# Optimization experiments

Measured on AMD Instinct MI355X. Metric: run time of the kernel, lower is better.

## Reference

```python
import jax, jax.numpy as jnp
import numpy as np

CONF = 0.25      # confidence threshold (module default)
IOU = 0.45       # NMS IoU threshold (class attribute)
TOPK = 1000      # fixed candidate budget (jit-friendly stand-in for boolean filtering)
MAX_WH = 4096.0  # class offset so NMS is per-class (YOLOv5 trick)


def xywh2xyxy(b):
    xy, wh = b[..., :2], b[..., 2:4]
    return jnp.concatenate([xy - wh * 0.5, xy + wh * 0.5], axis=-1)


def box_iou(a, b):
    # a: [K,4] xyxy, b: [K,4] xyxy -> [K,K]
    lt = jnp.maximum(a[:, None, :2], b[None, :, :2])
    rb = jnp.minimum(a[:, None, 2:], b[None, :, 2:])
    wh = jnp.clip(rb - lt, 0.0)
    inter = wh[..., 0] * wh[..., 1]
    area_a = (a[:, 2] - a[:, 0]) * (a[:, 3] - a[:, 1])
    area_b = (b[:, 2] - b[:, 0]) * (b[:, 3] - b[:, 1])
    return inter / (area_a[:, None] + area_b[None, :] - inter + 1e-9)


def nms_single(pred):
    # pred: [N, 5+C] = (xywh, obj, cls scores)
    boxes = xywh2xyxy(pred[:, :4])
    obj = pred[:, 4]
    cls = pred[:, 5:]
    cls_conf = jnp.max(cls, axis=-1)
    cls_id = jnp.argmax(cls, axis=-1)
    score = obj * cls_conf                       # conf = obj_conf * cls_conf
    masked = jnp.where(score > CONF, score, -1.0)
    top_scores, idx = jax.lax.top_k(masked, TOPK)  # sorted descending
    boxes_k = boxes[idx]                          # [K,4]
    cls_k = cls_id[idx].astype(boxes.dtype)       # [K]
    valid_k = top_scores > CONF                   # candidates passing threshold
    # per-class NMS via coordinate offset
    off = boxes_k + cls_k[:, None] * MAX_WH
    iou = box_iou(off, off)
    iou = iou * (1.0 - jnp.eye(TOPK, dtype=iou.dtype))  # ignore self-IoU
    # greedy suppression in descending score order
    def step(suppressed, i):
        keep_i = jnp.logical_and(jnp.logical_not(suppressed[i]), valid_k[i])
        suppressed = jnp.logical_or(suppressed, jnp.logical_and(keep_i, iou[i] > IOU))
        return suppressed, keep_i
    _, keep = jax.lax.scan(step, jnp.zeros(TOPK, dtype=bool), jnp.arange(TOPK))
    det = jnp.concatenate([boxes_k, top_scores[:, None], cls_k[:, None]], axis=-1)  # [K,6]
    return jnp.where(keep[:, None], det, 0.0)


def setup_inputs() -> dict:
    key = jax.random.key(0)
    x = jax.random.uniform(key, (8, 25200, 85), dtype=jnp.float32)
    return {"x": x}


def reference(x):
    # [B, K, 6] detections (xyxy, conf, cls); suppressed/invalid rows zeroed.
    return jax.vmap(nms_single)(x)
```

## Files before the change

kernel.cpp:

```cpp
#include <hip/hip_runtime.h>
#include <stdint.h>

#define NB 8
#define NPRED 25200
#define NTOP 1000
#define NCLS 80
#define CONF_T 0.25f
#define IOU_THR 0.45f
#define MAXWH 4096.0f
#define CAP 2048
#define NBINS2 8192
#define SBLK 128
#define SBPB 197

typedef unsigned long long u64;

__device__ __forceinline__ u64 shfl_xor_u64(u64 v, int m) {
    int lo = __shfl_xor((int)(unsigned)v, m);
    int hi = __shfl_xor((int)(unsigned)(v >> 32), m);
    return ((u64)(unsigned)hi << 32) | (unsigned)lo;
}
__device__ __forceinline__ u64 shfl_u64(u64 v, int src) {
    int lo = __shfl((int)(unsigned)v, src);
    int hi = __shfl((int)(unsigned)(v >> 32), src);
    return ((u64)(unsigned)hi << 32) | (unsigned)lo;
}

__global__ __launch_bounds__(256) void k_score(const float* __restrict__ x,
                                               float* __restrict__ msc,
                                               int* __restrict__ cls) {
#pragma clang fp contract(off)
    __shared__ __align__(16) float sm[SBLK * 85];
    const int b = blockIdx.x / SBPB;
    const int blk = blockIdx.x % SBPB;
    const int t = threadIdx.x;
    const int wave = t >> 6, lane = t & 63;
    const long long TOT4 = (long long)NB * NPRED * 85 / 4;
    const long long base4 = ((long long)b * NPRED + (long long)blk * SBLK) * 85 / 4;
    const float4* x4 = (const float4*)x;
    const int tile4 = SBLK * 85 / 4;

    for (int k = 0; k < 11; ++k) {
        int ib = k * 256 + wave * 64;
        int fi = ib + lane;
        if (fi < tile4) {
            long long gi = base4 + fi;
            if (gi >= TOT4) gi = TOT4 - 1;
            __builtin_amdgcn_global_load_lds(
                (const __attribute__((address_space(1))) void*)(x4 + gi),
                (__attribute__((address_space(3))) void*)(sm + (size_t)ib * 4),
                16, 0, 0);
        }
    }
    __syncthreads();

    const int p = t >> 1;
    const int h = t & 1;
    const int pred = blk * SBLK + p;
    const float* rowp = &sm[p * 85];
    float obj = rowp[4];
    const int cb = 5 + h * 40;
    float best = rowp[cb];
    int bid = h * 40;
    for (int c = 1; c < 40; ++c) {
        float v = rowp[cb + c];
        if (v > best) { best = v; bid = h * 40 + c; }
    }
    float obest = __shfl_xor(best, 1);
    int obid = __shfl_xor(bid, 1);
    if (h == 0 && pred < NPRED) {
        float fb = best; int fc = bid;
        if (obest > fb) { fb = obest; fc = obid; }
        float score = obj * fb;
        int q = b * NPRED + pred;
        msc[q] = (score > CONF_T) ? score : -1.0f;
        cls[q] = fc;
    }
}

__global__ __launch_bounds__(1024) void k_fused(const float* __restrict__ x,
                                                const float* __restrict__ msc,
                                                const int* __restrict__ cls,
                                                float* __restrict__ out) {
#pragma clang fp contract(off)
    __shared__ __align__(16) unsigned char uni[CAP * 8];
    __shared__ __align__(16) unsigned hh[NBINS2];
    __shared__ __align__(16) float4 obx[NTOP];
    __shared__ float oco[NTOP];
    __shared__ float osc[NTOP];
    __shared__ int   ocl[NTOP];
    __shared__ int sB;
    __shared__ unsigned lcnt;
    __shared__ int ovf;
    u64* keys = (u64*)uni;
    const int b = blockIdx.x, t = threadIdx.x;
    const float* ms = msc + (size_t)b * NPRED;

    float sv[25];
#pragma unroll
    for (int k = 0; k < 25; ++k) {
        int p = t + k * 1024;
        sv[k] = (p < NPRED) ? ms[p] : -1.0f;
    }

    for (int i = t; i < NBINS2; i += 1024) hh[i] = 0;
    if (t == 0) { lcnt = 0; ovf = 0; sB = 0; }
    __syncthreads();

#pragma unroll
    for (int k = 0; k < 25; ++k) {
        float s = sv[k];
        if (s > CONF_T) {
            unsigned bits = __float_as_uint(s);
            int bin = (int)(bits >> 11) - 0x7D000;
            bin = bin < 0 ? 0 : (bin > 8191 ? 8191 : bin);
            atomicAdd(&hh[bin], 1u);
        }
    }
    __syncthreads();

    unsigned* ctmp = (unsigned*)uni;
    {
        const uint4* h4 = (const uint4*)hh;
        uint4 a = h4[t * 2], d = h4[t * 2 + 1];
        ctmp[t] = a.x + a.y + a.z + a.w + d.x + d.y + d.z + d.w;
    }
    __syncthreads();

    if (t < 64) {
        const int lane = t;
        const int hi = 1023 - 16 * lane;
        unsigned lc[16];
        unsigned sum = 0;
#pragma unroll
        for (int k = 0; k < 16; ++k) { lc[k] = ctmp[hi - k]; sum += lc[k]; }
        unsigned v = sum;
        for (int d = 1; d < 64; d <<= 1) {
            unsigned o = __shfl_up(v, d);
            if (lane >= d) v += o;
        }
        unsigned excl = v - sum;
        u64 ball = __ballot(v >= NTOP);
        if (ball != 0) {
            int sel = __builtin_ctzll(ball);
            if (lane == sel) {
                unsigned run = excl, runBefore = 0;
                int C = 0;
                for (int k = 0; k < 16; ++k) {
                    runBefore = run;
                    run += lc[k];
                    if (run >= NTOP) { C = hi - k; break; }
                }
                const uint4* f4 = (const uint4*)&hh[C * 8];
                uint4 fa = f4[0], fb = f4[1];
                unsigned fbin[8] = {fa.x, fa.y, fa.z, fa.w, fb.x, fb.y, fb.z, fb.w};
                unsigned run2 = runBefore;
                int Bf = C * 8;
                for (int ff = 7; ff >= 0; --ff) {
                    run2 += fbin[ff];
                    if (run2 >= NTOP) { Bf = C * 8 + ff; break; }
                }
                sB = Bf;
            }
        }
    }
    __syncthreads();
    const int B = sB;

#pragma unroll
    for (int k = 0; k < 25; ++k) {
        float s = sv[k];
        if (s > CONF_T) {
            unsigned bits = __float_as_uint(s);
            int bin = (int)(bits >> 11) - 0x7D000;
            bin = bin < 0 ? 0 : (bin > 8191 ? 8191 : bin);
            if (bin >= B) {
                unsigned slot = atomicAdd(&lcnt, 1u);
                if (slot < CAP)
                    keys[slot] = ((u64)(~bits) << 32) | (unsigned)(t + k * 1024);
            }
        }
    }
    __syncthreads();
    unsigned c = lcnt; if (c > CAP) c = CAP;
    const bool fastSort = (c <= 1024u);
    const unsigned PAD = fastSort ? 1024u : (unsigned)CAP;
    for (unsigned i = c + t; i < PAD; i += 1024) keys[i] = ~0ULL;
    __syncthreads();

    if (fastSort) {
        u64 v = keys[t];
        for (unsigned k = 2; k <= 64; k <<= 1)
            for (unsigned j = k >> 1; j >= 1; j >>= 1) {
                u64 pv = shfl_xor_u64(v, (int)j);
                bool asc = (((unsigned)t & k) == 0u);
                bool lower = (((unsigned)t & j) == 0u);
                bool tm = (asc == lower);
                v = ((v < pv) == tm) ? v : pv;
            }
        for (unsigned k = 128; k <= 1024; k <<= 1) {
            for (unsigned j = k >> 1; j >= 64; j >>= 1) {
                keys[t] = v;
                __syncthreads();
                u64 pv = keys[(unsigned)t ^ j];
                bool asc = (((unsigned)t & k) == 0u);
                bool lower = (((unsigned)t & j) == 0u);
                bool tm = (asc == lower);
                v = ((v < pv) == tm) ? v : pv;
                __syncthreads();
            }
            for (unsigned j = 32; j >= 1; j >>= 1) {
                u64 pv = shfl_xor_u64(v, (int)j);
                bool asc = (((unsigned)t & k) == 0u);
                bool lower = (((unsigned)t & j) == 0u);
                bool tm = (asc == lower);
                v = ((v < pv) == tm) ? v : pv;
            }
        }
        keys[t] = v;
        __syncthreads();
    } else {
        const unsigned ia = (((unsigned)t & ~63u) << 1) | ((unsigned)t & 63u);
        const unsigned ib = ia + 64u;
        auto ce = [&](u64& v, unsigned i, unsigned j, unsigned k) {
            u64 pv = shfl_xor_u64(v, (int)j);
            bool asc = ((i & k) == 0u);
            bool lower = ((i & j) == 0u);
            bool takeMin = (asc == lower);
            bool less = (v < pv);
            v = (takeMin == less) ? v : pv;
        };
        {
            u64 a = keys[ia], d = keys[ib];
            for (unsigned k = 2; k <= 64; k <<= 1)
                for (unsigned j = k >> 1; j >= 1; j >>= 1) {
                    ce(a, ia, j, k);
                    ce(d, ib, j, k);
                }
            keys[ia] = a; keys[ib] = d;
        }
        __syncthreads();
        for (unsigned k = 128; k <= CAP; k <<= 1) {
            for (unsigned j = k >> 1; j >= 64; j >>= 1) {
                unsigned i = (((unsigned)t & ~(j - 1)) << 1) | ((unsigned)t & (j - 1));
                unsigned pi = i | j;
                bool up = ((i & k) == 0);
                u64 a = keys[i], d = keys[pi];
                bool sw = up ? (a > d) : (a < d);
                if (sw) { keys[i] = d; keys[pi] = a; }
                __syncthreads();
            }
            u64 a = keys[ia], d = keys[ib];
            for (unsigned j = 32; j >= 1; j >>= 1) {
                ce(a, ia, j, k);
                ce(d, ib, j, k);
            }
            keys[ia] = a; keys[ib] = d;
            __syncthreads();
        }
    }

    if (t < NTOP) {
        u64 key = keys[t];
        unsigned p = (unsigned)key;
        float score = __uint_as_float(~(unsigned)(key >> 32));
        bool v = score > CONF_T;
        float4 o = make_float4(0.f, 0.f, 0.f, 0.f);
        float co = 0.f; int cid = -1;
        if (v) {
            const float* xp = x + ((size_t)b * NPRED + p) * 85;
            float xc = xp[0], yc = xp[1], w = xp[2], h = xp[3];
            float hw = w * 0.5f, hh2 = h * 0.5f;
            o.x = xc - hw; o.y = yc - hh2; o.z = xc + hw; o.w = yc + hh2;
            cid = cls[(size_t)b * NPRED + p];
            co = (float)cid * MAXWH;
        }
        obx[t] = o; oco[t] = co; osc[t] = score; ocl[t] = cid;
    }
    __syncthreads();

    u64* bm = (u64*)uni;
    unsigned char* sup = uni + 10240;
    for (int i = t; i < NCLS * 16; i += 1024) bm[i] = 0;
    if (t < NTOP) sup[t] = 0;
    __syncthreads();
    if (t < NTOP && ocl[t] >= 0)
        atomicOr(&bm[ocl[t] * 16 + (t >> 6)], 1ull << (t & 63));
    __syncthreads();

    {
        const int waveId = t >> 6, lane2 = t & 63;
        for (int c2 = waveId; c2 < NCLS; c2 += 16) {
            u64 w = (lane2 < 16) ? bm[c2 * 16 + lane2] : 0ull;
            int cum = 0, myw = -1, rem = 0;
            u64 myword = 0;
#pragma unroll
            for (int ww = 0; ww < 16; ++ww) {
                u64 wv = shfl_u64(w, ww);
                int pc = __popcll(wv);
                if (myw < 0 && lane2 < cum + pc) { myw = ww; rem = lane2 - cum; myword = wv; }
                cum += pc;
            }
            int n2 = cum;
            if (n2 == 0) continue;
            if (n2 > 64) { ovf = 1; continue; }
            bool active = (lane2 < n2);
            int rank = 0;
            float ax1v = 0.f, ay1v = 0.f, ax2v = 0.f, ay2v = 0.f, arv = 0.f;
            if (active) {
                int pos = 0, r = rem;
#pragma unroll
                for (int wd = 32; wd >= 1; wd >>= 1) {
                    u64 mask = ((1ull << wd) - 1ull) << pos;
                    int cc = __popcll(myword & mask);
                    if (r >= cc) { r -= cc; pos += wd; }
                }
                rank = myw * 64 + pos;
                float4 A = obx[rank]; float cA = oco[rank];
                ax1v = A.x + cA; ay1v = A.y + cA;
                ax2v = A.z + cA; ay2v = A.w + cA;
                arv = (ax2v - ax1v) * (ay2v - ay1v);
            }
            u64 alive = (n2 >= 64) ? ~0ull : ((1ull << n2) - 1ull);
            u64 kept = 0;
            while (alive) {
                int i = (int)__builtin_ctzll(alive);
                u64 bit = 1ull << i;
                kept |= bit;
                float bx1 = __shfl(ax1v, i), by1 = __shfl(ay1v, i);
                float bx2 = __shfl(ax2v, i), by2 = __shfl(ay2v, i);
                float bar = __shfl(arv, i);
                float ltx = fmaxf(bx1, ax1v), lty = fmaxf(by1, ay1v);
                float rbx = fminf(bx2, ax2v), rby = fminf(by2, ay2v);
                float ww2 = fmaxf(rbx - ltx, 0.0f), hh3 = fmaxf(rby - lty, 0.0f);
                float inter = ww2 * hh3;
                float iou = inter / (((bar + arv) - inter) + 1e-9f);
                u64 suppr = __ballot(iou > IOU_THR);
                alive &= ~(suppr | bit);
            }
            if (active) sup[rank] = ((kept >> lane2) & 1ull) ? 0 : 1;
        }
    }
    __syncthreads();

    if (ovf && t == 0) {
        for (int c2 = 0; c2 < NCLS; ++c2) {
            int n2 = 0;
            for (int w2 = 0; w2 < 16; ++w2) n2 += __popcll(bm[c2 * 16 + w2]);
            if (n2 <= 64) continue;
            for (int a2 = 0; a2 < NTOP; ++a2) {
                if (ocl[a2] != c2 || sup[a2]) continue;
                float4 A = obx[a2]; float cA = oco[a2];
                float ax1 = A.x + cA, ay1 = A.y + cA;
                float ax2 = A.z + cA, ay2 = A.w + cA;
                float areaA = (ax2 - ax1) * (ay2 - ay1);
                for (int d2 = a2 + 1; d2 < NTOP; ++d2) {
                    if (ocl[d2] != c2 || sup[d2]) continue;
                    float4 Bb = obx[d2];
                    float bx1 = Bb.x + cA, by1 = Bb.y + cA;
                    float bx2 = Bb.z + cA, by2 = Bb.w + cA;
                    float ltx = fmaxf(ax1, bx1), lty = fmaxf(ay1, by1);
                    float rbx = fminf(ax2, bx2), rby = fminf(ay2, by2);
                    float ww = fmaxf(rbx - ltx, 0.0f), hh3 = fmaxf(rby - lty, 0.0f);
                    float inter = ww * hh3;
                    float areaB = (bx2 - bx1) * (by2 - by1);
                    float iou = inter / (((areaA + areaB) - inter) + 1e-9f);
                    if (iou > IOU_THR) sup[d2] = 1;
                }
            }
        }
    }
    __syncthreads();

    if (t < NTOP) {
        bool keep = (ocl[t] >= 0) && (sup[t] == 0);
        float4 o = obx[t];
        size_t d6 = ((size_t)b * NTOP + t) * 6;
        out[d6 + 0] = keep ? o.x : 0.0f;
        out[d6 + 1] = keep ? o.y : 0.0f;
        out[d6 + 2] = keep ? o.z : 0.0f;
        out[d6 + 3] = keep ? o.w : 0.0f;
        out[d6 + 4] = keep ? osc[t] : 0.0f;
        out[d6 + 5] = keep ? (float)ocl[t] : 0.0f;
    }
}

extern "C" void kernel_launch(void* const* d_in, const int* in_sizes, int n_in,
                              void* d_out, int out_size, void* d_ws, size_t ws_size,
                              hipStream_t stream) {
    const float* x = (const float*)d_in[0];
    char* ws = (char*)d_ws;
    float* msc = (float*)(ws);
    int* cls = (int*)(ws + 806400);

    k_score<<<NB * SBPB, 256, 0, stream>>>(x, msc, cls);
    k_fused<<<NB, 1024, 0, stream>>>(x, msc, cls, (float*)d_out);
}
```

Measured before the change: 134.0 us.

## Replace threshold-select and bitonic sort with histogram counting sort

Top-k selection now uses a block-wide suffix scan over a 4096-bin score histogram. Each candidate is scattered straight to its slot via per-bin atomic offsets, and entries within a bin are then ordered by a small insertion sort. This removes the threshold-bin search, the candidate compaction and the bitonic sort with its many block barriers. In exchange it relies on bins holding few items, since each insertion sort runs serially, and on the top 1000 fitting in the first 2048 key slots.

```diff
diff --git a/kernel.cpp b/kernel.cpp
--- a/kernel.cpp
+++ b/kernel.cpp
@@ -8,18 +8,15 @@
 #define CONF_T 0.25f
 #define IOU_THR 0.45f
 #define MAXWH 4096.0f
-#define CAP 2048
-#define NBINS2 8192
+#define NKEYS 2048
+#define NBINSF 4096
+#define FSH 12
+#define FBASE 0x3E800
 #define SBLK 128
 #define SBPB 197
 
 typedef unsigned long long u64;
 
-__device__ __forceinline__ u64 shfl_xor_u64(u64 v, int m) {
-    int lo = __shfl_xor((int)(unsigned)v, m);
-    int hi = __shfl_xor((int)(unsigned)(v >> 32), m);
-    return ((u64)(unsigned)hi << 32) | (unsigned)lo;
-}
 __device__ __forceinline__ u64 shfl_u64(u64 v, int src) {
     int lo = __shfl((int)(unsigned)v, src);
     int hi = __shfl((int)(unsigned)(v >> 32), src);
@@ -83,17 +80,17 @@
                                                 const int* __restrict__ cls,
                                                 float* __restrict__ out) {
 #pragma clang fp contract(off)
-    __shared__ __align__(16) unsigned char uni[CAP * 8];
-    __shared__ __align__(16) unsigned hh[NBINS2];
+    __shared__ __align__(16) unsigned char uni[NKEYS * 8];
+    __shared__ __align__(16) unsigned hh[NBINSF];
+    __shared__ unsigned wtot[16];
     __shared__ __align__(16) float4 obx[NTOP];
     __shared__ float oco[NTOP];
     __shared__ float osc[NTOP];
     __shared__ int   ocl[NTOP];
-    __shared__ int sB;
-    __shared__ unsigned lcnt;
     __shared__ int ovf;
     u64* keys = (u64*)uni;
     const int b = blockIdx.x, t = threadIdx.x;
+    const int wave = t >> 6, lane = t & 63;
     const float* ms = msc + (size_t)b * NPRED;
 
     float sv[25];
@@ -103,8 +100,8 @@
         sv[k] = (p < NPRED) ? ms[p] : -1.0f;
     }
 
-    for (int i = t; i < NBINS2; i += 1024) hh[i] = 0;
-    if (t == 0) { lcnt = 0; ovf = 0; sB = 0; }
+    ((uint4*)hh)[t] = make_uint4(0u, 0u, 0u, 0u);
+    if (t == 0) ovf = 0;
     __syncthreads();
 
 #pragma unroll
@@ -112,162 +109,83 @@
         float s = sv[k];
         if (s > CONF_T) {
             unsigned bits = __float_as_uint(s);
-            int bin = (int)(bits >> 11) - 0x7D000;
-            bin = bin < 0 ? 0 : (bin > 8191 ? 8191 : bin);
+            int bin = (int)(bits >> FSH) - FBASE;
+            bin = bin < 0 ? 0 : (bin > NBINSF - 1 ? NBINSF - 1 : bin);
             atomicAdd(&hh[bin], 1u);
         }
     }
     __syncthreads();
 
-    unsigned* ctmp = (unsigned*)uni;
-    {
-        const uint4* h4 = (const uint4*)hh;
-        uint4 a = h4[t * 2], d = h4[t * 2 + 1];
-        ctmp[t] = a.x + a.y + a.z + a.w + d.x + d.y + d.z + d.w;
-    }
-    __syncthreads();
-
-    if (t < 64) {
-        const int lane = t;
-        const int hi = 1023 - 16 * lane;
-        unsigned lc[16];
-        unsigned sum = 0;
-#pragma unroll
-        for (int k = 0; k < 16; ++k) { lc[k] = ctmp[hi - k]; sum += lc[k]; }
-        unsigned v = sum;
-        for (int d = 1; d < 64; d <<= 1) {
-            unsigned o = __shfl_up(v, d);
-            if (lane >= d) v += o;
-        }
-        unsigned excl = v - sum;
-        u64 ball = __ballot(v >= NTOP);
-        if (ball != 0) {
-            int sel = __builtin_ctzll(ball);
-            if (lane == sel) {
-                unsigned run = excl, runBefore = 0;
-                int C = 0;
-                for (int k = 0; k < 16; ++k) {
-                    runBefore = run;
-                    run += lc[k];
-                    if (run >= NTOP) { C = hi - k; break; }
-                }
-                const uint4* f4 = (const uint4*)&hh[C * 8];
-                uint4 fa = f4[0], fb = f4[1];
-                unsigned fbin[8] = {fa.x, fa.y, fa.z, fa.w, fb.x, fb.y, fb.z, fb.w};
-                unsigned run2 = runBefore;
-                int Bf = C * 8;
-                for (int ff = 7; ff >= 0; --ff) {
-                    run2 += fbin[ff];
-                    if (run2 >= NTOP) { Bf = C * 8 + ff; break; }
-                }
-                sB = Bf;
-            }
-        }
-    }
-    __syncthreads();
-    const int B = sB;
+    uint4 hc = ((const uint4*)hh)[t];
+    unsigned psum = hc.x + hc.y + hc.z + hc.w;
+    unsigned v = psum;
+    for (int d = 1; d < 64; d <<= 1) {
+        unsigned o = __shfl_down(v, d);
+        if (lane + d < 64) v += o;
+    }
+    if (lane == 0) wtot[wave] = v;
+    keys[t] = ~0ULL; keys[t + 1024] = ~0ULL;
+    __syncthreads();
+    unsigned after = 0;
+    for (int w2 = wave + 1; w2 < 16; ++w2) after += wtot[w2];
+    unsigned exclSuf = after + (v - psum);
+    unsigned o3 = exclSuf;
+    unsigned o2 = o3 + hc.w;
+    unsigned o1 = o2 + hc.z;
+    unsigned o0 = o1 + hc.y;
+    ((uint4*)hh)[t] = make_uint4(o0, o1, o2, o3);
+    __syncthreads();
 
 #pragma unroll
     for (int k = 0; k < 25; ++k) {
         float s = sv[k];
         if (s > CONF_T) {
             unsigned bits = __float_as_uint(s);
-            int bin = (int)(bits >> 11) - 0x7D000;
-            bin = bin < 0 ? 0 : (bin > 8191 ? 8191 : bin);
-            if (bin >= B) {
-                unsigned slot = atomicAdd(&lcnt, 1u);
-                if (slot < CAP)
-                    keys[slot] = ((u64)(~bits) << 32) | (unsigned)(t + k * 1024);
-            }
-        }
-    }
-    __syncthreads();
-    unsigned c = lcnt; if (c > CAP) c = CAP;
-    const bool fastSort = (c <= 1024u);
-    const unsigned PAD = fastSort ? 1024u : (unsigned)CAP;
-    for (unsigned i = c + t; i < PAD; i += 1024) keys[i] = ~0ULL;
-    __syncthreads();
-
-    if (fastSort) {
-        u64 v = keys[t];
-        for (unsigned k = 2; k <= 64; k <<= 1)
-            for (unsigned j = k >> 1; j >= 1; j >>= 1) {
-                u64 pv = shfl_xor_u64(v, (int)j);
-                bool asc = (((unsigned)t & k) == 0u);
-                bool lower = (((unsigned)t & j) == 0u);
-                bool tm = (asc == lower);
-                v = ((v < pv) == tm) ? v : pv;
-            }
-        for (unsigned k = 128; k <= 1024; k <<= 1) {
-            for (unsigned j = k >> 1; j >= 64; j >>= 1) {
-                keys[t] = v;
-                __syncthreads();
-                u64 pv = keys[(unsigned)t ^ j];
-                bool asc = (((unsigned)t & k) == 0u);
-                bool lower = (((unsigned)t & j) == 0u);
-                bool tm = (asc == lower);
-                v = ((v < pv) == tm) ? v : pv;
-                __syncthreads();
-            }
-            for (unsigned j = 32; j >= 1; j >>= 1) {
-                u64 pv = shfl_xor_u64(v, (int)j);
-                bool asc = (((unsigned)t & k) == 0u);
-                bool lower = (((unsigned)t & j) == 0u);
-                bool tm = (asc == lower);
-                v = ((v < pv) == tm) ? v : pv;
-            }
-        }
-        keys[t] = v;
-        __syncthreads();
-    } else {
-        const unsigned ia = (((unsigned)t & ~63u) << 1) | ((unsigned)t & 63u);
-        const unsigned ib = ia + 64u;
-        auto ce = [&](u64& v, unsigned i, unsigned j, unsigned k) {
-            u64 pv = shfl_xor_u64(v, (int)j);
-            bool asc = ((i & k) == 0u);
-            bool lower = ((i & j) == 0u);
-            bool takeMin = (asc == lower);
-            bool less = (v < pv);
-            v = (takeMin == less) ? v : pv;
-        };
-        {
-            u64 a = keys[ia], d = keys[ib];
-            for (unsigned k = 2; k <= 64; k <<= 1)
-                for (unsigned j = k >> 1; j >= 1; j >>= 1) {
-                    ce(a, ia, j, k);
-                    ce(d, ib, j, k);
-                }
-            keys[ia] = a; keys[ib] = d;
-        }
-        __syncthreads();
-        for (unsigned k = 128; k <= CAP; k <<= 1) {
-            for (unsigned j = k >> 1; j >= 64; j >>= 1) {
-                unsigned i = (((unsigned)t & ~(j - 1)) << 1) | ((unsigned)t & (j - 1));
-                unsigned pi = i | j;
-                bool up = ((i & k) == 0);
-                u64 a = keys[i], d = keys[pi];
-                bool sw = up ? (a > d) : (a < d);
-                if (sw) { keys[i] = d; keys[pi] = a; }
-                __syncthreads();
-            }
-            u64 a = keys[ia], d = keys[ib];
-            for (unsigned j = 32; j >= 1; j >>= 1) {
-                ce(a, ia, j, k);
-                ce(d, ib, j, k);
-            }
-            keys[ia] = a; keys[ib] = d;
-            __syncthreads();
-        }
-    }
+            int bin = (int)(bits >> FSH) - FBASE;
+            bin = bin < 0 ? 0 : (bin > NBINSF - 1 ? NBINSF - 1 : bin);
+            unsigned slot = atomicAdd(&hh[bin], 1u);
+            if (slot < (unsigned)NKEYS)
+                keys[slot] = ((u64)(~bits) << 32) | (unsigned)(t + k * 1024);
+        }
+    }
+    __syncthreads();
+
+    auto binOf = [](u64 kk) -> int {
+        unsigned bits = ~(unsigned)(kk >> 32);
+        int bin = (int)(bits >> FSH) - FBASE;
+        return bin < 0 ? 0 : (bin > NBINSF - 1 ? NBINSF - 1 : bin);
+    };
+#pragma unroll
+    for (int pp = 0; pp < 2; ++pp) {
+        int p = t + pp * 1024;
+        u64 k0 = keys[p];
+        if (k0 == ~0ULL) continue;
+        int mybin = binOf(k0);
+        bool head = (p == 0) || (keys[p - 1] == ~0ULL) || (binOf(keys[p - 1]) != mybin);
+        if (!head) continue;
+        int e = p + 1;
+        while (e < NKEYS) {
+            u64 kn = keys[e];
+            if (kn == ~0ULL || binOf(kn) != mybin) break;
+            ++e;
+        }
+        for (int i2 = p + 1; i2 < e; ++i2) {
+            u64 kv = keys[i2];
+            int j2 = i2 - 1;
+            while (j2 >= p && keys[j2] > kv) { keys[j2 + 1] = keys[j2]; --j2; }
+            keys[j2 + 1] = kv;
+        }
+    }
+    __syncthreads();
 
     if (t < NTOP) {
         u64 key = keys[t];
         unsigned p = (unsigned)key;
         float score = __uint_as_float(~(unsigned)(key >> 32));
-        bool v = score > CONF_T;
+        bool vd = score > CONF_T;
         float4 o = make_float4(0.f, 0.f, 0.f, 0.f);
         float co = 0.f; int cid = -1;
-        if (v) {
+        if (vd) {
             const float* xp = x + ((size_t)b * NPRED + p) * 85;
             float xc = xp[0], yc = xp[1], w = xp[2], h = xp[3];
             float hw = w * 0.5f, hh2 = h * 0.5f;
@@ -289,22 +207,21 @@
     __syncthreads();
 
     {
-        const int waveId = t >> 6, lane2 = t & 63;
-        for (int c2 = waveId; c2 < NCLS; c2 += 16) {
-            u64 w = (lane2 < 16) ? bm[c2 * 16 + lane2] : 0ull;
+        for (int c2 = wave; c2 < NCLS; c2 += 16) {
+            u64 w = (lane < 16) ? bm[c2 * 16 + lane] : 0ull;
             int cum = 0, myw = -1, rem = 0;
             u64 myword = 0;
 #pragma unroll
             for (int ww = 0; ww < 16; ++ww) {
                 u64 wv = shfl_u64(w, ww);
                 int pc = __popcll(wv);
-                if (myw < 0 && lane2 < cum + pc) { myw = ww; rem = lane2 - cum; myword = wv; }
+                if (myw < 0 && lane < cum + pc) { myw = ww; rem = lane - cum; myword = wv; }
                 cum += pc;
             }
             int n2 = cum;
             if (n2 == 0) continue;
             if (n2 > 64) { ovf = 1; continue; }
-            bool active = (lane2 < n2);
+            bool active = (lane < n2);
             int rank = 0;
             float ax1v = 0.f, ay1v = 0.f, ax2v = 0.f, ay2v = 0.f, arv = 0.f;
             if (active) {
@@ -338,7 +255,7 @@
                 u64 suppr = __ballot(iou > IOU_THR);
                 alive &= ~(suppr | bit);
             }
-            if (active) sup[rank] = ((kept >> lane2) & 1ull) ? 0 : 1;
+            if (active) sup[rank] = ((kept >> lane) & 1ull) ? 0 : 1;
         }
     }
     __syncthreads();
```

Measured after the change: 145.0 us. 8.2% more time.
